# Kernel optimization log

Hardware: AMD Instinct MI355X
Metric: run time of the kernel (lower is better)

## Reference

```python
import jax, jax.numpy as jnp
import numpy as np

KERNEL = 5
STRIDE = 1
PAD = 2


def _unfold(x, k, stride, pad):
    # torch.nn.functional.unfold: (N,C,H,W) -> (N, C*k*k, h_out*w_out),
    # feature dim ordered (c, kh, kw) slowest-to-fastest.
    n, c, h, w = x.shape
    xp = jnp.pad(x, ((0, 0), (0, 0), (pad, pad), (pad, pad)))
    h_out = (h - k + 2 * pad) // stride + 1
    w_out = (w - k + 2 * pad) // stride + 1
    cols = jnp.stack(
        [xp[:, :, di:di + stride * h_out:stride, dj:dj + stride * w_out:stride]
         for di in range(k) for dj in range(k)],
        axis=2,
    )  # (n, c, k*k, h_out, w_out)
    return cols.reshape(n, c * k * k, h_out * w_out), h_out, w_out


def setup_inputs() -> dict:
    key = jax.random.key(0)
    kx, kw = jax.random.split(key)
    x = jax.random.normal(kx, (8, 3, 64, 64), dtype=jnp.float32)
    W = jax.random.normal(kw, (64, 3, KERNEL, KERNEL), dtype=jnp.float32)
    return {"x": x, "W": W}


def reference(x, W):
    n_filters, c, kh, kw = W.shape
    n = x.shape[0]
    xc, h_out, w_out = _unfold(x, kh, STRIDE, PAD)          # (n, D, P)
    # match torch: permute(1,2,0).view(D, P*n)  -> column index = p*n + i
    X_col = jnp.transpose(xc, (1, 2, 0)).reshape(xc.shape[1], -1)  # (D, M)
    W_col = W.reshape(n_filters, -1)                         # (F, D)
    # -1/2 ||x - w||^2 = -1/2 ||x||^2 - 1/2 ||w||^2 + w.x  (GEMM form,
    # avoids the (F, D, M) broadcast tensor the torch code materializes)
    x2 = jnp.sum(X_col * X_col, axis=0)                      # (M,)
    w2 = jnp.sum(W_col * W_col, axis=1)                      # (F,)
    out = W_col @ X_col - 0.5 * (x2[None, :] + w2[:, None])  # (F, M)
    out = out.reshape(n_filters, h_out, w_out, n)
    return jnp.transpose(out, (3, 0, 1, 2))                  # (n, F, h_out, w_out)
```

## Files before the change

### kernel.cpp

```cpp
#include <hip/hip_runtime.h>


#define CH   3
#define NF   64
#define KK   5
#define PADC 2
#define HH   64
#define WW   64

#define NROWS (CH * KK)
#define ROWW  68
#define WSTRIDE 124

__global__ __launch_bounds__(256) void euclid_conv_kernel(
    const float* __restrict__ x,
    const float* __restrict__ Wt,
    float* __restrict__ out)
{
    __shared__ float xs[NROWS * ROWW];
    __shared__ float ws[NF * WSTRIDE];
    __shared__ float w2s[NF];

    const int t   = threadIdx.x;
    const int blk = blockIdx.x;
    const int n   = blk >> 6;
    const int y   = blk & 63;

    for (int idx = t; idx < NROWS * ROWW; idx += 256) {
        int row_id = idx / ROWW;
        int col    = idx - row_id * ROWW;
        int c  = row_id / KK;
        int kh = row_id - c * KK;
        int r  = y + kh - PADC;
        int cx = col - PADC;
        float v = 0.0f;
        if ((unsigned)r < HH && (unsigned)cx < WW)
            v = x[((n * CH + c) * HH + r) * WW + cx];
        xs[idx] = v;
    }

    for (int idx = t; idx < NF * 75; idx += 256) {
        int f = idx / 75;
        int d = idx - f * 75;
        int c   = d / 25;
        int rem = d - c * 25;
        int kh  = rem / 5;
        int kw  = rem - kh * 5;
        ws[f * WSTRIDE + (c * KK + kh) * 8 + kw] = Wt[idx];
    }
    __syncthreads();

    if (t < NF) {
        float s = 0.0f;
        const float* wf = &ws[t * WSTRIDE];
        #pragma unroll
        for (int rr = 0; rr < NROWS; ++rr)
            #pragma unroll
            for (int kw = 0; kw < KK; ++kw) {
                float w = wf[rr * 8 + kw];
                s += w * w;
            }
        w2s[t] = s;
    }

    const int p4 = t & 15;
    const int f4 = t >> 4;
    const int x0 = p4 * 4;
    const int fb = f4 * 4;

    float acc[4][4];
    #pragma unroll
    for (int j = 0; j < 4; ++j)
        #pragma unroll
        for (int i = 0; i < 4; ++i)
            acc[j][i] = 0.0f;
    float ps2[4] = {0.0f, 0.0f, 0.0f, 0.0f};

    #pragma unroll
    for (int rr = 0; rr < NROWS; ++rr) {
        const float4 wlo = *(const float4*)&xs[rr * ROWW + x0];
        const float4 whi = *(const float4*)&xs[rr * ROWW + x0 + 4];
        float win[8] = {wlo.x, wlo.y, wlo.z, wlo.w,
                        whi.x, whi.y, whi.z, whi.w};

        #pragma unroll
        for (int i = 0; i < 4; ++i)
            #pragma unroll
            for (int kw = 0; kw < KK; ++kw)
                ps2[i] += win[i + kw] * win[i + kw];

        #pragma unroll
        for (int j = 0; j < 4; ++j) {
            const float4 w03 = *(const float4*)&ws[(fb + j) * WSTRIDE + rr * 8];
            const float  w4  = ws[(fb + j) * WSTRIDE + rr * 8 + 4];
            const float wv[5] = {w03.x, w03.y, w03.z, w03.w, w4};
            #pragma unroll
            for (int i = 0; i < 4; ++i)
                #pragma unroll
                for (int kw = 0; kw < KK; ++kw)
                    acc[j][i] += wv[kw] * win[i + kw];
        }
    }

    __syncthreads();

    #pragma unroll
    for (int j = 0; j < 4; ++j) {
        const float wsq = w2s[fb + j];
        float4 o;
        o.x = acc[j][0] - 0.5f * (ps2[0] + wsq);
        o.y = acc[j][1] - 0.5f * (ps2[1] + wsq);
        o.z = acc[j][2] - 0.5f * (ps2[2] + wsq);
        o.w = acc[j][3] - 0.5f * (ps2[3] + wsq);
        *(float4*)&out[((n * NF + fb + j) * HH + y) * WW + x0] = o;
    }
}

extern "C" void kernel_launch(void* const* d_in, const int* in_sizes, int n_in,
                              void* d_out, int out_size, void* d_ws, size_t ws_size,
                              hipStream_t stream) {
    const float* x  = (const float*)d_in[0];
    const float* Wt = (const float*)d_in[1];
    float* out = (float*)d_out;
    (void)in_sizes; (void)n_in; (void)out_size; (void)d_ws; (void)ws_size;

    dim3 grid(8 * 64);
    dim3 block(256);
    hipLaunchKernelGGL(euclid_conv_kernel, grid, block, 0, stream, x, Wt, out);
}
```

Measured before the change: 65.35 us.

## Split filters across two blocks and precompute patch norms cooperatively in shared memory

Doubles the grid so each block handles half of the 64 filters for one output row, which raises the block count on the many-CU GPU and halves the per-block weight staging. Per-pixel squared norms are now computed once per block in shared memory, instead of redundantly by each thread. The thread tile changes from 4 filters x 4 pixels to 1 filter x 8 pixels. The cost is that the input row window is loaded twice (once per half), there is an extra barrier, and there is less register reuse of the input window across filters.

```diff
diff --git a/kernel.cpp b/kernel.cpp
--- a/kernel.cpp
+++ b/kernel.cpp
@@ -10,6 +10,7 @@
 
 #define NROWS (CH * KK)
 #define ROWW  68
+#define BLKF  32
 #define WSTRIDE 124
 
 __global__ __launch_bounds__(256) void euclid_conv_kernel(
@@ -18,13 +19,17 @@
     float* __restrict__ out)
 {
     __shared__ float xs[NROWS * ROWW];
-    __shared__ float ws[NF * WSTRIDE];
-    __shared__ float w2s[NF];
+    __shared__ float ws[BLKF * WSTRIDE];
+    __shared__ float rs[NROWS * WW];
+    __shared__ float ps2s[WW];
+    __shared__ float w2s[BLKF];
 
-    const int t   = threadIdx.x;
-    const int blk = blockIdx.x;
-    const int n   = blk >> 6;
-    const int y   = blk & 63;
+    const int t    = threadIdx.x;
+    const int blk  = blockIdx.x;
+    const int n    = blk >> 7;
+    const int rem  = blk & 127;
+    const int y    = rem >> 1;
+    const int half = rem & 1;
 
     for (int idx = t; idx < NROWS * ROWW; idx += 256) {
         int row_id = idx / ROWW;
@@ -39,20 +44,35 @@
         xs[idx] = v;
     }
 
-    for (int idx = t; idx < NF * 75; idx += 256) {
+    for (int idx = t; idx < BLKF * 75; idx += 256) {
         int f = idx / 75;
         int d = idx - f * 75;
         int c   = d / 25;
-        int rem = d - c * 25;
-        int kh  = rem / 5;
-        int kw  = rem - kh * 5;
-        ws[f * WSTRIDE + (c * KK + kh) * 8 + kw] = Wt[idx];
+        int r2  = d - c * 25;
+        int kh  = r2 / 5;
+        int kw  = r2 - kh * 5;
+        ws[f * WSTRIDE + (c * KK + kh) * 8 + kw] = Wt[(half * BLKF + f) * 75 + d];
     }
     __syncthreads();
 
-    if (t < NF) {
+    for (int idx = t; idx < NROWS * WW; idx += 256) {
+        int rr = idx >> 6;
+        int xx = idx & 63;
+        const float* p = &xs[rr * ROWW + xx];
+        rs[idx] = p[0]*p[0] + p[1]*p[1] + p[2]*p[2] + p[3]*p[3] + p[4]*p[4];
+    }
+    __syncthreads();
+
+    if (t < WW) {
         float s = 0.0f;
-        const float* wf = &ws[t * WSTRIDE];
+        #pragma unroll
+        for (int rr = 0; rr < NROWS; ++rr)
+            s += rs[rr * WW + t];
+        ps2s[t] = s;
+    } else if (t < WW + BLKF) {
+        int f = t - WW;
+        float s = 0.0f;
+        const float* wf = &ws[f * WSTRIDE];
         #pragma unroll
         for (int rr = 0; rr < NROWS; ++rr)
             #pragma unroll
@@ -60,60 +80,54 @@
                 float w = wf[rr * 8 + kw];
                 s += w * w;
             }
-        w2s[t] = s;
+        w2s[f] = s;
     }
 
-    const int p4 = t & 15;
-    const int f4 = t >> 4;
-    const int x0 = p4 * 4;
-    const int fb = f4 * 4;
+    const int p8 = t & 7;
+    const int fl = t >> 3;
+    const int x0 = p8 * 8;
 
-    float acc[4][4];
+    float acc[8];
     #pragma unroll
-    for (int j = 0; j < 4; ++j)
-        #pragma unroll
-        for (int i = 0; i < 4; ++i)
-            acc[j][i] = 0.0f;
-    float ps2[4] = {0.0f, 0.0f, 0.0f, 0.0f};
+    for (int i = 0; i < 8; ++i) acc[i] = 0.0f;
 
     #pragma unroll
     for (int rr = 0; rr < NROWS; ++rr) {
-        const float4 wlo = *(const float4*)&xs[rr * ROWW + x0];
-        const float4 whi = *(const float4*)&xs[rr * ROWW + x0 + 4];
-        float win[8] = {wlo.x, wlo.y, wlo.z, wlo.w,
-                        whi.x, whi.y, whi.z, whi.w};
-
+        const float4 a = *(const float4*)&xs[rr * ROWW + x0];
+        const float4 b = *(const float4*)&xs[rr * ROWW + x0 + 4];
+        const float4 c4 = *(const float4*)&xs[rr * ROWW + x0 + 8];
+        const float win[12] = {a.x, a.y, a.z, a.w,
+                               b.x, b.y, b.z, b.w,
+                               c4.x, c4.y, c4.z, c4.w};
+        const float4 w03 = *(const float4*)&ws[fl * WSTRIDE + rr * 8];
+        const float  w4  = ws[fl * WSTRIDE + rr * 8 + 4];
+        const float wv[5] = {w03.x, w03.y, w03.z, w03.w, w4};
         #pragma unroll
-        for (int i = 0; i < 4; ++i)
+        for (int i = 0; i < 8; ++i)
             #pragma unroll
             for (int kw = 0; kw < KK; ++kw)
-                ps2[i] += win[i + kw] * win[i + kw];
-
-        #pragma unroll
-        for (int j = 0; j < 4; ++j) {
-            const float4 w03 = *(const float4*)&ws[(fb + j) * WSTRIDE + rr * 8];
-            const float  w4  = ws[(fb + j) * WSTRIDE + rr * 8 + 4];
-            const float wv[5] = {w03.x, w03.y, w03.z, w03.w, w4};
-            #pragma unroll
-            for (int i = 0; i < 4; ++i)
-                #pragma unroll
-                for (int kw = 0; kw < KK; ++kw)
-                    acc[j][i] += wv[kw] * win[i + kw];
-        }
+                acc[i] += wv[kw] * win[i + kw];
     }
 
     __syncthreads();
 
-    #pragma unroll
-    for (int j = 0; j < 4; ++j) {
-        const float wsq = w2s[fb + j];
-        float4 o;
-        o.x = acc[j][0] - 0.5f * (ps2[0] + wsq);
-        o.y = acc[j][1] - 0.5f * (ps2[1] + wsq);
-        o.z = acc[j][2] - 0.5f * (ps2[2] + wsq);
-        o.w = acc[j][3] - 0.5f * (ps2[3] + wsq);
-        *(float4*)&out[((n * NF + fb + j) * HH + y) * WW + x0] = o;
-    }
+    const float wsq = w2s[fl];
+    const float4 q0 = *(const float4*)&ps2s[x0];
+    const float4 q1 = *(const float4*)&ps2s[x0 + 4];
+    const int f = half * BLKF + fl;
+    float* op = &out[((n * NF + f) * HH + y) * WW + x0];
+
+    float4 o0, o1;
+    o0.x = acc[0] - 0.5f * (q0.x + wsq);
+    o0.y = acc[1] - 0.5f * (q0.y + wsq);
+    o0.z = acc[2] - 0.5f * (q0.z + wsq);
+    o0.w = acc[3] - 0.5f * (q0.w + wsq);
+    o1.x = acc[4] - 0.5f * (q1.x + wsq);
+    o1.y = acc[5] - 0.5f * (q1.y + wsq);
+    o1.z = acc[6] - 0.5f * (q1.z + wsq);
+    o1.w = acc[7] - 0.5f * (q1.w + wsq);
+    *(float4*)&op[0] = o0;
+    *(float4*)&op[4] = o1;
 }
 
 extern "C" void kernel_launch(void* const* d_in, const int* in_sizes, int n_in,
@@ -124,7 +138,7 @@
     float* out = (float*)d_out;
     (void)in_sizes; (void)n_in; (void)out_size; (void)d_ws; (void)ws_size;
 
-    dim3 grid(8 * 64);
+    dim3 grid(8 * 64 * 2);
     dim3 block(256);
     hipLaunchKernelGGL(euclid_conv_kernel, grid, block, 0, stream, x, Wt, out);
 }
```

After: 67.33 us. +3.0%, slower.
